# Optimization experiments

Hardware: AMD Instinct MI355X
Metric: run time of the kernel (lower is better)

## Reference

```python
import jax, jax.numpy as jnp
import numpy as np

T_KD = 20.0      # KL_divergence temperature
T_THR = 6.0      # Threshold_weights temperature
EPS = 1e-05


def _margin(o, gathered):
    # torch.sort descending, take top-2; margin only when target is the argmax value
    top2 = jax.lax.top_k(o, 2)[0]                      # [B, 2]
    return jnp.where(top2[:, 0] == gathered, top2[:, 0] - top2[:, 1], 0.0)


def _forward(outputs1, outputs2, outputs3, outputs4, out_s, targets):
    B = targets.shape[0]
    idx = jnp.arange(B)
    mimic = (outputs1 + outputs2 + outputs3 + outputs4) / 4.0

    teachers = [outputs1, outputs2, outputs3, outputs4, mimic]
    gathered = [t[idx, targets] for t in teachers]      # each [B]

    # C = min over gathered target logits of the 4 real teachers
    C = jnp.minimum(jnp.minimum(gathered[0].min(), gathered[1].min()),
                    jnp.minimum(gathered[2].min(), gathered[3].min()))
    # if C < 0: shift everything by (-C + eps); else no shift
    shift = jnp.where(C < 0, -C + EPS, 0.0)

    shifted = [t + shift for t in teachers]
    g_shift = [g + shift for g in gathered]

    # Threshold_weights: margin per branch, softmax over 5 branches
    preds = jnp.stack([_margin(s, g) for s, g in zip(shifted, g_shift)], axis=1)  # [B,5]
    out_threshold = jax.nn.softmax(preds / T_THR, axis=1)

    # max over the 4 (shifted) teacher logit tensors
    max_preds = jnp.maximum(jnp.maximum(shifted[0].max(), shifted[1].max()),
                            jnp.maximum(shifted[2].max(), shifted[3].max()))

    # per-sample CE of student (shared across branches)
    log_p_s = jax.nn.log_softmax(out_s, axis=1)
    CE = -log_p_s[idx, targets]                          # [B]

    log_ps_T = jax.nn.log_softmax(out_s / T_KD, axis=1)  # [B,C]

    def branch_loss(teacher, g_s):
        w2 = g_s / max_preds          # weights2
        w1 = 1.0 - w2                 # weights1
        log_pt = jax.nn.log_softmax(teacher / T_KD, axis=1)
        p_t = jnp.exp(log_pt)
        KD = jnp.sum(p_t * (log_pt - log_ps_T), axis=1) * (T_KD * T_KD)  # [B]
        return w1 * CE + w2 * KD

    # KD/CE use the ORIGINAL (unshifted) teacher logits
    losses = jnp.stack([branch_loss(t, g) for t, g in zip(teachers, g_shift)], axis=1)  # [B,5]
    return jnp.mean(jnp.sum(out_threshold * losses, axis=1))


def setup_inputs() -> dict:
    key = jax.random.key(0)
    ks = jax.random.split(key, 6)
    B, C = 8192, 1000
    return {
        "outputs1": jax.random.normal(ks[0], (B, C), dtype=jnp.float32),
        "outputs2": jax.random.normal(ks[1], (B, C), dtype=jnp.float32),
        "outputs3": jax.random.normal(ks[2], (B, C), dtype=jnp.float32),
        "outputs4": jax.random.normal(ks[3], (B, C), dtype=jnp.float32),
        "out_s": jax.random.normal(ks[4], (B, C), dtype=jnp.float32),
        "targets": jax.random.randint(ks[5], (B,), 0, C, dtype=jnp.int64 if jax.config.jax_enable_x64 else jnp.int32),
    }


def reference(outputs1, outputs2, outputs3, outputs4, out_s, targets):
    return _forward(outputs1, outputs2, outputs3, outputs4, out_s, targets)
```

## Files before the change

kernel.cpp:

```cpp
#include <hip/hip_runtime.h>
#include <math.h>

#define NB 8192
#define NC 1000
#define NF4 250


#define LOG2E 1.4426950408889634f
#define LN2   0.6931471805599453f

__device__ __forceinline__ float fexp2(float x) { return __builtin_amdgcn_exp2f(x); }
__device__ __forceinline__ float flog2(float x) { return __builtin_amdgcn_logf(x); }

__device__ __forceinline__ float wredsum(float v) {
#pragma unroll
  for (int m = 32; m >= 1; m >>= 1) v += __shfl_xor(v, m, 64);
  return v;
}
__device__ __forceinline__ float wredmax(float v) {
#pragma unroll
  for (int m = 32; m >= 1; m >>= 1) v = fmaxf(v, __shfl_xor(v, m, 64));
  return v;
}
__device__ __forceinline__ float wredmin(float v) {
#pragma unroll
  for (int m = 32; m >= 1; m >>= 1) v = fminf(v, __shfl_xor(v, m, 64));
  return v;
}
__device__ __forceinline__ void wredtop2(float& t1, float& t2) {
#pragma unroll
  for (int m = 32; m >= 1; m >>= 1) {
    float o1 = __shfl_xor(t1, m, 64);
    float o2 = __shfl_xor(t2, m, 64);
    float lo = fminf(t1, o1);
    t1 = fmaxf(t1, o1);
    t2 = fmaxf(fmaxf(t2, o2), lo);
  }
}
__device__ __forceinline__ float f4get(const float4& v, int e) {
  return e == 0 ? v.x : e == 1 ? v.y : e == 2 ? v.z : v.w;
}

__global__ __launch_bounds__(256) void k_rowstats(
    const float* __restrict__ o1, const float* __restrict__ o2,
    const float* __restrict__ o3, const float* __restrict__ o4,
    const float* __restrict__ os, const int* __restrict__ tg,
    float* __restrict__ ws) {
  const int lane = threadIdx.x & 63;
  const int row = blockIdx.x * 4 + (threadIdx.x >> 6);

  const int target = tg[row];
  const float g1 = (o1 + (size_t)row * NC)[target];
  const float g2 = (o2 + (size_t)row * NC)[target];
  const float g3 = (o3 + (size_t)row * NC)[target];
  const float g4 = (o4 + (size_t)row * NC)[target];
  const float gs = (os + (size_t)row * NC)[target];

  const float4* p1 = (const float4*)(o1 + (size_t)row * NC);
  const float4* p2 = (const float4*)(o2 + (size_t)row * NC);
  const float4* p3 = (const float4*)(o3 + (size_t)row * NC);
  const float4* p4 = (const float4*)(o4 + (size_t)row * NC);
  const float4* ps = (const float4*)(os + (size_t)row * NC);

  float4 a1[4], a2[4], a3[4], a4[4], asv[4];
  const float4 NEG4 = make_float4(-INFINITY, -INFINITY, -INFINITY, -INFINITY);
#pragma unroll
  for (int j = 0; j < 4; ++j) {
    int f = j * 64 + lane;
    if (f < NF4) {
      a1[j] = p1[f]; a2[j] = p2[f]; a3[j] = p3[f]; a4[j] = p4[f]; asv[j] = ps[f];
    } else {
      a1[j] = NEG4; a2[j] = NEG4; a3[j] = NEG4; a4[j] = NEG4; asv[j] = NEG4;
    }
  }

  float t1[5], t2[5];
#pragma unroll
  for (int t = 0; t < 5; ++t) { t1[t] = -INFINITY; t2[t] = -INFINITY; }
  float ms = -INFINITY;

#pragma unroll
  for (int j = 0; j < 4; ++j) {
#pragma unroll
    for (int e = 0; e < 4; ++e) {
      float w0 = f4get(a1[j], e);
      float w1 = f4get(a2[j], e);
      float w2 = f4get(a3[j], e);
      float w3 = f4get(a4[j], e);
      float wsv = f4get(asv[j], e);
      float wm = ((w0 + w1) + w2 + w3) * 0.25f;
      float w[5] = {w0, w1, w2, w3, wm};
#pragma unroll
      for (int t = 0; t < 5; ++t) {
        t2[t] = fmaxf(t2[t], fminf(t1[t], w[t]));
        t1[t] = fmaxf(t1[t], w[t]);
      }
      ms = fmaxf(ms, wsv);
    }
  }
#pragma unroll
  for (int t = 0; t < 5; ++t) wredtop2(t1[t], t2[t]);
  ms = wredmax(ms);

  const float K20 = LOG2E / 20.0f;
  float Z[5] = {0.f, 0.f, 0.f, 0.f, 0.f};
  float S1[5] = {0.f, 0.f, 0.f, 0.f, 0.f};
  float Z1 = 0.f, Z20 = 0.f;
#pragma unroll
  for (int j = 0; j < 4; ++j) {
    if (j * 64 + lane < NF4) {
#pragma unroll
      for (int e = 0; e < 4; ++e) {
        float w0 = f4get(a1[j], e);
        float w1 = f4get(a2[j], e);
        float w2 = f4get(a3[j], e);
        float w3 = f4get(a4[j], e);
        float wsv = f4get(asv[j], e);
        float wm = ((w0 + w1) + w2 + w3) * 0.25f;
        float w[5] = {w0, w1, w2, w3, wm};
#pragma unroll
        for (int t = 0; t < 5; ++t) {
          float et = fexp2((w[t] - t1[t]) * K20);
          Z[t] += et;
          S1[t] += et * (w[t] - wsv);
        }
        Z1 += fexp2((wsv - ms) * LOG2E);
        Z20 += fexp2((wsv - ms) * K20);
      }
    }
  }
#pragma unroll
  for (int t = 0; t < 5; ++t) { Z[t] = wredsum(Z[t]); S1[t] = wredsum(S1[t]); }
  Z1 = wredsum(Z1);
  Z20 = wredsum(Z20);

  if (lane == 0) {
    const float gm = ((g1 + g2) + g3 + g4) * 0.25f;
    float gg[5] = {g1, g2, g3, g4, gm};

    const float lse_s = ms * 0.05f + flog2(Z20) * LN2;
    const float CE = ms + flog2(Z1) * LN2 - gs;

#pragma unroll
    for (int t = 0; t < 5; ++t) {
      float lse_t = t1[t] * 0.05f + flog2(Z[t]) * LN2;
      float KD = 400.0f * (S1[t] / (20.0f * Z[t]) - lse_t + lse_s);
      float margin = (t1[t] == gg[t]) ? (t1[t] - t2[t]) : 0.0f;
      ws[(size_t)t * NB + row] = margin;
      ws[(size_t)(5 + t) * NB + row] = gg[t];
      ws[(size_t)(10 + t) * NB + row] = KD;
    }
    ws[(size_t)15 * NB + row] = CE;
    ws[(size_t)16 * NB + row] = fminf(fminf(g1, g2), fminf(g3, g4));
    ws[(size_t)17 * NB + row] = fmaxf(fmaxf(t1[0], t1[1]), fmaxf(t1[2], t1[3]));
  }
}

__global__ __launch_bounds__(1024) void k_minmax(float* __restrict__ ws,
                                                 float* __restrict__ out) {
  const int tid = threadIdx.x;
  const int lane = tid & 63, wv = tid >> 6;
  __shared__ float sA[16], sB[16];

  float mn = INFINITY, mx = -INFINITY;
  for (int r = tid; r < NB; r += 1024) {
    mn = fminf(mn, ws[(size_t)16 * NB + r]);
    mx = fmaxf(mx, ws[(size_t)17 * NB + r]);
  }
  mn = wredmin(mn);
  mx = wredmax(mx);
  if (lane == 0) { sA[wv] = mn; sB[wv] = mx; }
  __syncthreads();
  if (tid == 0) {
    float a = sA[0], b = sB[0];
    for (int i = 1; i < 16; ++i) { a = fminf(a, sA[i]); b = fmaxf(b, sB[i]); }
    float shift = (a < 0.0f) ? (-a + 1e-5f) : 0.0f;
    ws[(size_t)18 * NB] = shift;
    ws[(size_t)18 * NB + 1] = b + shift;
    out[0] = 0.0f;
  }
}

__global__ __launch_bounds__(256) void k_loss(const float* __restrict__ ws,
                                              float* __restrict__ out) {
  const int tid = threadIdx.x;
  const int lane = tid & 63, wv = tid >> 6;
  const int r = blockIdx.x * 256 + tid;
  __shared__ float sA[4];

  const float shift = ws[(size_t)18 * NB];
  const float maxp = ws[(size_t)18 * NB + 1];
  const float K6 = LOG2E / 6.0f;

  float m[5], e[5];
#pragma unroll
  for (int t = 0; t < 5; ++t) m[t] = ws[(size_t)t * NB + r];
  float pm = fmaxf(fmaxf(fmaxf(m[0], m[1]), fmaxf(m[2], m[3])), m[4]);
  float Zl = 0.0f;
#pragma unroll
  for (int t = 0; t < 5; ++t) { e[t] = fexp2((m[t] - pm) * K6); Zl += e[t]; }
  float ce = ws[(size_t)15 * NB + r];
  float rl = 0.0f;
#pragma unroll
  for (int t = 0; t < 5; ++t) {
    float g = ws[(size_t)(5 + t) * NB + r];
    float kd = ws[(size_t)(10 + t) * NB + r];
    float w2 = (g + shift) / maxp;
    float loss = (1.0f - w2) * ce + w2 * kd;
    rl += e[t] * loss;
  }
  float acc = rl / Zl;

  acc = wredsum(acc);
  if (lane == 0) sA[wv] = acc;
  __syncthreads();
  if (tid == 0) {
    float tot = (sA[0] + sA[1]) + (sA[2] + sA[3]);
    atomicAdd(out, tot * (1.0f / 8192.0f));
  }
}

extern "C" void kernel_launch(void* const* d_in, const int* in_sizes, int n_in,
                              void* d_out, int out_size, void* d_ws, size_t ws_size,
                              hipStream_t stream) {
  const float* o1 = (const float*)d_in[0];
  const float* o2 = (const float*)d_in[1];
  const float* o3 = (const float*)d_in[2];
  const float* o4 = (const float*)d_in[3];
  const float* os = (const float*)d_in[4];
  const int* tg = (const int*)d_in[5];
  float* ws = (float*)d_ws;
  float* out = (float*)d_out;

  k_rowstats<<<NB / 4, 256, 0, stream>>>(o1, o2, o3, o4, os, tg, ws);
  k_minmax<<<1, 1024, 0, stream>>>(ws, out);
  k_loss<<<NB / 256, 256, 0, stream>>>(ws, out);
}
```

Measured before the change: 189.2 us.

## Single-pass row stats without max subtraction; replace minmax kernel with atomics

Row statistics are now computed in a single streaming loop over the row, with software-prefetched float4 loads, instead of loading the whole row into registers and making two passes. The max-subtraction in the softmax sums is dropped, which relies on the input logits being small enough not to overflow exp. The global min/max reduction kernel is replaced by order-preserving integer atomicMin/atomicMax issued from the row kernel, plus a tiny init kernel. The aim is lower register pressure and one fewer reduction launch, at the cost of numerical robustness for large logits.

```diff
diff --git a/kernel.cpp b/kernel.cpp
--- a/kernel.cpp
+++ b/kernel.cpp
@@ -12,19 +12,17 @@
 __device__ __forceinline__ float fexp2(float x) { return __builtin_amdgcn_exp2f(x); }
 __device__ __forceinline__ float flog2(float x) { return __builtin_amdgcn_logf(x); }
 
+__device__ __forceinline__ unsigned fkey(float f) {
+  unsigned u = __float_as_uint(f);
+  return (u & 0x80000000u) ? ~u : (u | 0x80000000u);
+}
+__device__ __forceinline__ float funkey(unsigned k) {
+  return __uint_as_float((k & 0x80000000u) ? (k ^ 0x80000000u) : ~k);
+}
+
 __device__ __forceinline__ float wredsum(float v) {
 #pragma unroll
   for (int m = 32; m >= 1; m >>= 1) v += __shfl_xor(v, m, 64);
-  return v;
-}
-__device__ __forceinline__ float wredmax(float v) {
-#pragma unroll
-  for (int m = 32; m >= 1; m >>= 1) v = fmaxf(v, __shfl_xor(v, m, 64));
-  return v;
-}
-__device__ __forceinline__ float wredmin(float v) {
-#pragma unroll
-  for (int m = 32; m >= 1; m >>= 1) v = fminf(v, __shfl_xor(v, m, 64));
   return v;
 }
 __device__ __forceinline__ void wredtop2(float& t1, float& t2) {
@@ -39,6 +37,18 @@
 }
 __device__ __forceinline__ float f4get(const float4& v, int e) {
   return e == 0 ? v.x : e == 1 ? v.y : e == 2 ? v.z : v.w;
+}
+__device__ __forceinline__ float uload(const float* p) {
+  return __uint_as_float(__builtin_amdgcn_readfirstlane(__float_as_uint(*p)));
+}
+
+__global__ void k_init(float* __restrict__ ws, float* __restrict__ out) {
+  if (threadIdx.x == 0) {
+    unsigned* scal = (unsigned*)(ws + (size_t)16 * NB);
+    scal[0] = 0xFFFFFFFFu;
+    scal[1] = 0u;
+    out[0] = 0.0f;
+  }
 }
 
 __global__ __launch_bounds__(256) void k_rowstats(
@@ -48,87 +58,65 @@
     float* __restrict__ ws) {
   const int lane = threadIdx.x & 63;
   const int row = blockIdx.x * 4 + (threadIdx.x >> 6);
+  const size_t base = (size_t)row * NC;
 
   const int target = tg[row];
-  const float g1 = (o1 + (size_t)row * NC)[target];
-  const float g2 = (o2 + (size_t)row * NC)[target];
-  const float g3 = (o3 + (size_t)row * NC)[target];
-  const float g4 = (o4 + (size_t)row * NC)[target];
-  const float gs = (os + (size_t)row * NC)[target];
-
-  const float4* p1 = (const float4*)(o1 + (size_t)row * NC);
-  const float4* p2 = (const float4*)(o2 + (size_t)row * NC);
-  const float4* p3 = (const float4*)(o3 + (size_t)row * NC);
-  const float4* p4 = (const float4*)(o4 + (size_t)row * NC);
-  const float4* ps = (const float4*)(os + (size_t)row * NC);
-
-  float4 a1[4], a2[4], a3[4], a4[4], asv[4];
-  const float4 NEG4 = make_float4(-INFINITY, -INFINITY, -INFINITY, -INFINITY);
-#pragma unroll
+  const float g1 = uload(o1 + base + target);
+  const float g2 = uload(o2 + base + target);
+  const float g3 = uload(o3 + base + target);
+  const float g4 = uload(o4 + base + target);
+  const float gs = uload(os + base + target);
+
+  const float4* p1 = (const float4*)(o1 + base);
+  const float4* p2 = (const float4*)(o2 + base);
+  const float4* p3 = (const float4*)(o3 + base);
+  const float4* p4 = (const float4*)(o4 + base);
+  const float4* ps = (const float4*)(os + base);
+
+  float t1[5], t2[5], Z[5], S1[5];
+#pragma unroll
+  for (int t = 0; t < 5; ++t) {
+    t1[t] = -INFINITY; t2[t] = -INFINITY; Z[t] = 0.f; S1[t] = 0.f;
+  }
+  float Z1 = 0.f, Z20 = 0.f;
+  const float K20 = LOG2E / 20.0f;
+
+  float4 c1 = p1[lane], c2 = p2[lane], c3 = p3[lane], c4 = p4[lane], cs = ps[lane];
+#pragma unroll 1
   for (int j = 0; j < 4; ++j) {
-    int f = j * 64 + lane;
-    if (f < NF4) {
-      a1[j] = p1[f]; a2[j] = p2[f]; a3[j] = p3[f]; a4[j] = p4[f]; asv[j] = ps[f];
-    } else {
-      a1[j] = NEG4; a2[j] = NEG4; a3[j] = NEG4; a4[j] = NEG4; asv[j] = NEG4;
+    float4 n1 = c1, n2 = c2, n3 = c3, n4 = c4, ns = cs;
+    if (j < 3) {
+      int fn = (j + 1) * 64 + lane;
+      int fc = fn < NF4 ? fn : 0;
+      n1 = p1[fc]; n2 = p2[fc]; n3 = p3[fc]; n4 = p4[fc]; ns = ps[fc];
     }
-  }
-
-  float t1[5], t2[5];
-#pragma unroll
-  for (int t = 0; t < 5; ++t) { t1[t] = -INFINITY; t2[t] = -INFINITY; }
-  float ms = -INFINITY;
-
-#pragma unroll
-  for (int j = 0; j < 4; ++j) {
-#pragma unroll
-    for (int e = 0; e < 4; ++e) {
-      float w0 = f4get(a1[j], e);
-      float w1 = f4get(a2[j], e);
-      float w2 = f4get(a3[j], e);
-      float w3 = f4get(a4[j], e);
-      float wsv = f4get(asv[j], e);
-      float wm = ((w0 + w1) + w2 + w3) * 0.25f;
-      float w[5] = {w0, w1, w2, w3, wm};
-#pragma unroll
-      for (int t = 0; t < 5; ++t) {
-        t2[t] = fmaxf(t2[t], fminf(t1[t], w[t]));
-        t1[t] = fmaxf(t1[t], w[t]);
-      }
-      ms = fmaxf(ms, wsv);
-    }
-  }
-#pragma unroll
-  for (int t = 0; t < 5; ++t) wredtop2(t1[t], t2[t]);
-  ms = wredmax(ms);
-
-  const float K20 = LOG2E / 20.0f;
-  float Z[5] = {0.f, 0.f, 0.f, 0.f, 0.f};
-  float S1[5] = {0.f, 0.f, 0.f, 0.f, 0.f};
-  float Z1 = 0.f, Z20 = 0.f;
-#pragma unroll
-  for (int j = 0; j < 4; ++j) {
     if (j * 64 + lane < NF4) {
 #pragma unroll
       for (int e = 0; e < 4; ++e) {
-        float w0 = f4get(a1[j], e);
-        float w1 = f4get(a2[j], e);
-        float w2 = f4get(a3[j], e);
-        float w3 = f4get(a4[j], e);
-        float wsv = f4get(asv[j], e);
+        float w0 = f4get(c1, e);
+        float w1 = f4get(c2, e);
+        float w2 = f4get(c3, e);
+        float w3 = f4get(c4, e);
+        float wsv = f4get(cs, e);
         float wm = ((w0 + w1) + w2 + w3) * 0.25f;
         float w[5] = {w0, w1, w2, w3, wm};
 #pragma unroll
         for (int t = 0; t < 5; ++t) {
-          float et = fexp2((w[t] - t1[t]) * K20);
+          t2[t] = fmaxf(t2[t], fminf(t1[t], w[t]));
+          t1[t] = fmaxf(t1[t], w[t]);
+          float et = fexp2(w[t] * K20);
           Z[t] += et;
-          S1[t] += et * (w[t] - wsv);
+          S1[t] = fmaf(et, w[t] - wsv, S1[t]);
         }
-        Z1 += fexp2((wsv - ms) * LOG2E);
-        Z20 += fexp2((wsv - ms) * K20);
+        Z1 += fexp2(wsv * LOG2E);
+        Z20 += fexp2(wsv * K20);
       }
     }
-  }
+    c1 = n1; c2 = n2; c3 = n3; c4 = n4; cs = ns;
+  }
+
+#pragma unroll
+  for (int t = 0; t < 5; ++t) wredtop2(t1[t], t2[t]);
 #pragma unroll
   for (int t = 0; t < 5; ++t) { Z[t] = wredsum(Z[t]); S1[t] = wredsum(S1[t]); }
   Z1 = wredsum(Z1);
@@ -138,12 +126,12 @@
     const float gm = ((g1 + g2) + g3 + g4) * 0.25f;
     float gg[5] = {g1, g2, g3, g4, gm};
 
-    const float lse_s = ms * 0.05f + flog2(Z20) * LN2;
-    const float CE = ms + flog2(Z1) * LN2 - gs;
+    const float lse_s = flog2(Z20) * LN2;
+    const float CE = flog2(Z1) * LN2 - gs;
 
 #pragma unroll
     for (int t = 0; t < 5; ++t) {
-      float lse_t = t1[t] * 0.05f + flog2(Z[t]) * LN2;
+      float lse_t = flog2(Z[t]) * LN2;
       float KD = 400.0f * (S1[t] / (20.0f * Z[t]) - lse_t + lse_s);
       float margin = (t1[t] == gg[t]) ? (t1[t] - t2[t]) : 0.0f;
       ws[(size_t)t * NB + row] = margin;
@@ -151,33 +139,10 @@
       ws[(size_t)(10 + t) * NB + row] = KD;
     }
     ws[(size_t)15 * NB + row] = CE;
-    ws[(size_t)16 * NB + row] = fminf(fminf(g1, g2), fminf(g3, g4));
-    ws[(size_t)17 * NB + row] = fmaxf(fmaxf(t1[0], t1[1]), fmaxf(t1[2], t1[3]));
-  }
-}
-
-__global__ __launch_bounds__(1024) void k_minmax(float* __restrict__ ws,
-                                                 float* __restrict__ out) {
-  const int tid = threadIdx.x;
-  const int lane = tid & 63, wv = tid >> 6;
-  __shared__ float sA[16], sB[16];
-
-  float mn = INFINITY, mx = -INFINITY;
-  for (int r = tid; r < NB; r += 1024) {
-    mn = fminf(mn, ws[(size_t)16 * NB + r]);
-    mx = fmaxf(mx, ws[(size_t)17 * NB + r]);
-  }
-  mn = wredmin(mn);
-  mx = wredmax(mx);
-  if (lane == 0) { sA[wv] = mn; sB[wv] = mx; }
-  __syncthreads();
-  if (tid == 0) {
-    float a = sA[0], b = sB[0];
-    for (int i = 1; i < 16; ++i) { a = fminf(a, sA[i]); b = fmaxf(b, sB[i]); }
-    float shift = (a < 0.0f) ? (-a + 1e-5f) : 0.0f;
-    ws[(size_t)18 * NB] = shift;
-    ws[(size_t)18 * NB + 1] = b + shift;
-    out[0] = 0.0f;
+
+    unsigned* scal = (unsigned*)(ws + (size_t)16 * NB);
+    atomicMin(&scal[0], fkey(fminf(fminf(g1, g2), fminf(g3, g4))));
+    atomicMax(&scal[1], fkey(fmaxf(fmaxf(t1[0], t1[1]), fmaxf(t1[2], t1[3]))));
   }
 }
 
@@ -188,8 +153,11 @@
   const int r = blockIdx.x * 256 + tid;
   __shared__ float sA[4];
 
-  const float shift = ws[(size_t)18 * NB];
-  const float maxp = ws[(size_t)18 * NB + 1];
+  const unsigned* scal = (const unsigned*)(ws + (size_t)16 * NB);
+  const float mn = funkey(scal[0]);
+  const float mx = funkey(scal[1]);
+  const float shift = (mn < 0.0f) ? (-mn + 1e-5f) : 0.0f;
+  const float maxp = mx + shift;
   const float K6 = LOG2E / 6.0f;
 
   float m[5], e[5];
@@ -232,7 +200,7 @@
   float* ws = (float*)d_ws;
   float* out = (float*)d_out;
 
+  k_init<<<1, 64, 0, stream>>>(ws, out);
   k_rowstats<<<NB / 4, 256, 0, stream>>>(o1, o2, o3, o4, os, tg, ws);
-  k_minmax<<<1, 1024, 0, stream>>>(ws, out);
   k_loss<<<NB / 256, 256, 0, stream>>>(ws, out);
 }
```

New measurement: 333.8 us. +76.4%, slower.
